# Kernel optimization log

Hardware: AMD Instinct MI355X
Metric: run time of the kernel (lower is better)

The kernel has to match this reference:

```python
import jax, jax.numpy as jnp
import numpy as np
import math

N_HEADS = 8

def setup_inputs() -> dict:
    key = jax.random.key(0)
    ks = jax.random.split(key, 5)
    B, S, D = 2, 2048, 512
    return {
        "x": jax.random.normal(ks[0], (B, S, D), dtype=jnp.float32),
        "w_in": jax.random.normal(ks[1], (3 * D, D), dtype=jnp.float32) * (1.0 / math.sqrt(D)),
        "b_in": jax.random.normal(ks[2], (3 * D,), dtype=jnp.float32) * 0.01,
        "w_out": jax.random.normal(ks[3], (D, D), dtype=jnp.float32) * (1.0 / math.sqrt(D)),
        "b_out": jax.random.normal(ks[4], (D,), dtype=jnp.float32) * 0.01,
        "casual_mask": 1,
    }

def reference(x, w_in, b_in, w_out, b_out, casual_mask):
    B, S, D = x.shape
    H = N_HEADS
    dh = D // H
    # in_proj: torch Linear -> x @ W.T + b
    qvk = x @ w_in.T + b_in  # [B, S, 3D]
    # NOTE: source unpacks as q, v, k (chunk order quirk preserved)
    q, v, k = jnp.split(qvk, 3, axis=-1)
    # [B, S, D] -> [B, H, S, dh]
    def to_heads(t):
        return t.reshape(B, S, H, dh).transpose(0, 2, 1, 3)
    q, k, v = to_heads(q), to_heads(k), to_heads(v)
    scores = jnp.einsum("bhqd,bhkd->bhqk", q, k)  # [B, H, S, S]
    if casual_mask:
        # mask BEFORE scaling, as in the source (-inf unaffected by division)
        tri = jnp.triu(jnp.ones((S, S), dtype=bool), k=1)
        scores = jnp.where(tri, -jnp.inf, scores)
    scores = scores / math.sqrt(dh)
    attn = jax.nn.softmax(scores, axis=-1)
    out = jnp.einsum("bhqk,bhkd->bhqd", attn, v)  # [B, H, S, dh]
    out = out.transpose(0, 2, 1, 3).reshape(B, S, D)
    return out @ w_out.T + b_out
```

## Files before the change

### kernel.cpp

```cpp
#include <hip/hip_runtime.h>
#include <hip/hip_bf16.h>

typedef unsigned short u16;
typedef unsigned int u32;
typedef __attribute__((ext_vector_type(8))) short bf16x8;
typedef __attribute__((ext_vector_type(4))) short bf16x4;
typedef __attribute__((ext_vector_type(4))) float f32x4;

#define DEVI __device__ __forceinline__

DEVI u16 f2bf(float f) {
  union { float f; unsigned int u; } v; v.f = f;
  unsigned int u = v.u;
  unsigned int r = (u + 0x7fffu + ((u >> 16) & 1u)) >> 16;
  return (u16)r;
}

DEVI float fexp2(float x) {
#if __has_builtin(__builtin_amdgcn_exp2f)
  return __builtin_amdgcn_exp2f(x);
#else
  return exp2f(x);
#endif
}

DEVI void lds_cp16(u16* lds, const u16* g) {
  __builtin_amdgcn_global_load_lds(
      (const __attribute__((address_space(1))) u32*)g,
      (__attribute__((address_space(3))) u32*)lds, 16, 0, 0);
}

DEVI f32x4 mfma16x16x16_bf16(bf16x4 a, bf16x4 b, f32x4 c) {
#if __has_builtin(__builtin_amdgcn_mfma_f32_16x16x16bf16_1k)
  return __builtin_amdgcn_mfma_f32_16x16x16bf16_1k(a, b, c, 0, 0, 0);
#else
  f32x4 d;
  asm volatile("v_mfma_f32_16x16x16_bf16 %0, %1, %2, %3"
               : "=v"(d) : "v"(a), "v"(b), "v"(c));
  return d;
#endif
}

__global__ __launch_bounds__(256) void cvt_all(
    const float4* __restrict__ x, const float4* __restrict__ wi,
    const float4* __restrict__ wo, u16* __restrict__ xb,
    u16* __restrict__ wib, u16* __restrict__ wob) {
  int i = blockIdx.x * 256 + threadIdx.x;
  const float4* src; u16* dst; int off;
  if (i < 524288)      { src = x;  dst = xb;  off = i; }
  else if (i < 720896) { src = wi; dst = wib; off = i - 524288; }
  else                 { src = wo; dst = wob; off = i - 720896; }
  float4 f = src[off];
  ushort4 o;
  o.x = f2bf(f.x); o.y = f2bf(f.y); o.z = f2bf(f.z); o.w = f2bf(f.w);
  ((ushort4*)dst)[off] = o;
}

__global__ __launch_bounds__(256) void inproj_gemm(
    const u16* __restrict__ xb, const u16* __restrict__ wb,
    const float* __restrict__ bin,
    u16* __restrict__ Qb, u16* __restrict__ Kb, u16* __restrict__ Vt) {
  const int K = 512;
  __shared__ u16 At[2][128 * 32];
  __shared__ u16 Bt[2][128 * 32];
  int tid = threadIdx.x;
  int w = tid >> 6, lane = tid & 63;
  int ql = lane & 15, quad = lane >> 4;
  int wr = w >> 1, wc = w & 1;
  int mtile = blockIdx.x * 128, ntile = blockIdx.y * 128;

  int r4 = lane >> 2, c4 = lane & 3;
  int swz4 = c4 ^ (r4 & 3);

  const u16* ag0 = xb + (size_t)(mtile + w * 32 + r4) * K + swz4 * 8;
  const u16* bg0 = wb + (size_t)(ntile + w * 32 + r4) * K + swz4 * 8;

  f32x4 acc[4][4];
#pragma unroll
  for (int t = 0; t < 4; ++t)
#pragma unroll
    for (int u = 0; u < 4; ++u) acc[t][u] = (f32x4){0, 0, 0, 0};

  lds_cp16(&At[0][w * 1024], ag0);
  lds_cp16(&At[0][w * 1024 + 512], ag0 + 16 * K);
  lds_cp16(&Bt[0][w * 1024], bg0);
  lds_cp16(&Bt[0][w * 1024 + 512], bg0 + 16 * K);

  int cb = ql & 3;
  for (int kk = 0; kk < 16; ++kk) {
    int cur = kk & 1;
    __syncthreads();
    if (kk < 15) {
      int k0 = (kk + 1) * 32;
      lds_cp16(&At[cur ^ 1][w * 1024], ag0 + k0);
      lds_cp16(&At[cur ^ 1][w * 1024 + 512], ag0 + 16 * K + k0);
      lds_cp16(&Bt[cur ^ 1][w * 1024], bg0 + k0);
      lds_cp16(&Bt[cur ^ 1][w * 1024 + 512], bg0 + 16 * K + k0);
    }
    bf16x8 af[4], bf[4];
#pragma unroll
    for (int t = 0; t < 4; ++t) {
      int row = wr * 64 + t * 16 + ql;
      af[t] = *(const bf16x8*)(&At[cur][row * 32 + ((quad ^ cb) * 8)]);
    }
#pragma unroll
    for (int u = 0; u < 4; ++u) {
      int row = wc * 64 + u * 16 + ql;
      bf[u] = *(const bf16x8*)(&Bt[cur][row * 32 + ((quad ^ cb) * 8)]);
    }
#pragma unroll
    for (int t = 0; t < 4; ++t)
#pragma unroll
      for (int u = 0; u < 4; ++u)
        acc[t][u] = __builtin_amdgcn_mfma_f32_16x16x32_bf16(af[t], bf[u], acc[t][u], 0, 0, 0);
  }

#pragma unroll
  for (int u = 0; u < 4; ++u) {
    int n = ntile + wc * 64 + u * 16 + ql;
    float bias = bin[n];
    int chunk = n >> 9;
    int nc = n & 511;
    int h = nc >> 6, d = nc & 63;
#pragma unroll
    for (int t = 0; t < 4; ++t)
#pragma unroll
      for (int r = 0; r < 4; ++r) {
        int m = mtile + wr * 64 + t * 16 + quad * 4 + r;
        int b = m >> 11, s = m & 2047;
        u16 val = f2bf(acc[t][u][r] + bias);
        int bh = b * 8 + h;
        if (chunk == 0)      Qb[((size_t)bh * 2048 + s) * 64 + d] = val;
        else if (chunk == 2) Kb[((size_t)bh * 2048 + s) * 64 + d] = val;
        else                 Vt[((size_t)bh * 64 + d) * 2048 + s] = val;
      }
  }
}

__global__ __launch_bounds__(512) void attn_kernel(
    const u16* __restrict__ Qb, const u16* __restrict__ Kb,
    const u16* __restrict__ Vt, u16* __restrict__ Ob) {
  const int S = 2048;
  __shared__ u16 Kt[2][2][4096];
  __shared__ u16 Vl[2][2][4096];
  int tid = threadIdx.x;
  int grp = tid >> 8;
  int w = (tid >> 6) & 3;
  int lane = tid & 63;
  int ql = lane & 15, quad = lane >> 4;
  int j = blockIdx.x;
  int tileA = j, tileB = 31 - j;
  int bh = blockIdx.y;
  int qbaseA = tileA * 64 + w * 16;
  int qbaseB = tileB * 64 + w * 16;
  const u16* Qh = Qb + (size_t)bh * S * 64;
  const u16* Kh = Kb + (size_t)bh * S * 64;
  const u16* Vh = Vt + (size_t)bh * 64 * S;

  int r8 = lane >> 3, c8 = lane & 7;
  int swz = c8 ^ r8;
  int cb = ql & 7;
  const float SCL = 0.180336878f;

  bf16x8 qA0 = *(const bf16x8*)(Qh + (size_t)(qbaseA + ql) * 64 + quad * 8);
  bf16x8 qA1 = *(const bf16x8*)(Qh + (size_t)(qbaseA + ql) * 64 + 32 + quad * 8);
  bf16x8 qB0 = *(const bf16x8*)(Qh + (size_t)(qbaseB + ql) * 64 + quad * 8);
  bf16x8 qB1 = *(const bf16x8*)(Qh + (size_t)(qbaseB + ql) * 64 + 32 + quad * 8);

  f32x4 oA[4] = {{0,0,0,0},{0,0,0,0},{0,0,0,0},{0,0,0,0}};
  f32x4 oB[4] = {{0,0,0,0},{0,0,0,0},{0,0,0,0},{0,0,0,0}};
  float mA = -3.0e38f, lA = 0.0f, mB = -3.0e38f, lB = 0.0f;

  auto stage = [&](int buf, int kbase) {
    const u16* kg = Kh + (size_t)(kbase + w * 16 + r8) * 64 + swz * 8;
    lds_cp16(&Kt[grp][buf][w * 1024], kg);
    lds_cp16(&Kt[grp][buf][w * 1024 + 512], kg + 8 * 64);
    const u16* vg = Vh + (size_t)(w * 16 + r8) * S + kbase + swz * 8;
    lds_cp16(&Vl[grp][buf][w * 1024], vg);
    lds_cp16(&Vl[grp][buf][w * 1024 + 512], vg + 8 * S);
  };
  auto process = [&](int cur, int kbase, int qbase, bf16x8 x0, bf16x8 x1,
                     f32x4 (&o)[4], float& m, float& l) {
    int q = qbase + ql;
    f32x4 st[4];
#pragma unroll
    for (int t = 0; t < 4; ++t) {
      const u16* kr = &Kt[grp][cur][(t * 16 + ql) * 64];
      bf16x8 kf0 = *(const bf16x8*)(kr + ((quad ^ cb) * 8));
      bf16x8 kf1 = *(const bf16x8*)(kr + (((quad + 4) ^ cb) * 8));
      f32x4 s = {0, 0, 0, 0};
      s = __builtin_amdgcn_mfma_f32_16x16x32_bf16(kf0, x0, s, 0, 0, 0);
      s = __builtin_amdgcn_mfma_f32_16x16x32_bf16(kf1, x1, s, 0, 0, 0);
      st[t] = s;
    }
    bool needmask = (kbase + 63 > qbase);
    float sc[4][4];
#pragma unroll
    for (int t = 0; t < 4; ++t)
#pragma unroll
      for (int r = 0; r < 4; ++r) {
        float v = st[t][r] * SCL;
        if (needmask) {
          int key = kbase + t * 16 + quad * 4 + r;
          if (key > q) v = -3.0e38f;
        }
        sc[t][r] = v;
      }
    float mx = sc[0][0];
#pragma unroll
    for (int t = 0; t < 4; ++t)
#pragma unroll
      for (int r = 0; r < 4; ++r) mx = fmaxf(mx, sc[t][r]);
    mx = fmaxf(mx, __shfl_xor(mx, 16));
    mx = fmaxf(mx, __shfl_xor(mx, 32));
    float mn = fmaxf(m, mx);
    float alpha = fexp2(m - mn);
    m = mn;
    float rs = 0.0f;
    bf16x4 p[4];
#pragma unroll
    for (int t = 0; t < 4; ++t)
#pragma unroll
      for (int r = 0; r < 4; ++r) {
        float e = fexp2(sc[t][r] - mn);
        rs += e;
        p[t][r] = (short)f2bf(e);
      }
    rs += __shfl_xor(rs, 16);
    rs += __shfl_xor(rs, 32);
    l = l * alpha + rs;
#pragma unroll
    for (int d = 0; d < 4; ++d) o[d] *= alpha;
#pragma unroll
    for (int t = 0; t < 4; ++t)
#pragma unroll
      for (int d = 0; d < 4; ++d) {
        const u16* vr = &Vl[grp][cur][(d * 16 + ql) * 64];
        bf16x4 vf = *(const bf16x4*)(vr + (((t * 2 + (quad >> 1)) ^ cb) * 8 + (quad & 1) * 4));
        o[d] = mfma16x16x16_bf16(vf, p[t], o[d]);
      }
  };

  {
    int i0 = grp * 17;
    int kb = (i0 <= tileA) ? i0 : (i0 - tileA - 1);
    stage(0, kb * 64);
  }

  for (int r = 0; r < 17; ++r) {
    int i = grp * 17 + r;
    int cur = r & 1;
    __syncthreads();
    int inext = i + 1;
    if (r + 1 < 17 && inext < 33) {
      int kb = (inext <= tileA) ? inext : (inext - tileA - 1);
      stage(cur ^ 1, kb * 64);
    }
    if (i < 33) {
      if (i <= tileA) process(cur, i * 64, qbaseA, qA0, qA1, oA, mA, lA);
      else            process(cur, (i - tileA - 1) * 64, qbaseB, qB0, qB1, oB, mB, lB);
    }
  }

  float* ob  = (float*)&Kt[0][0][0];
  float* mlb = (float*)&Vl[0][0][0];
  int lg = tid & 255;
  int b = bh >> 3, h = bh & 7;
  __syncthreads();
  if (grp == 1) {
#pragma unroll
    for (int d = 0; d < 4; ++d)
#pragma unroll
      for (int r = 0; r < 4; ++r) ob[lg * 16 + d * 4 + r] = oB[d][r];
    mlb[lg * 2] = mB;
    mlb[lg * 2 + 1] = lB;
  }
  __syncthreads();
  if (grp == 0) {
    float invA = 1.0f / lA;
    size_t rowA = ((size_t)b * 2048 + qbaseA + ql) * 512 + h * 64;
#pragma unroll
    for (int d = 0; d < 4; ++d) {
      ushort4 v;
      v.x = f2bf(oA[d][0] * invA);
      v.y = f2bf(oA[d][1] * invA);
      v.z = f2bf(oA[d][2] * invA);
      v.w = f2bf(oA[d][3] * invA);
      *(ushort4*)(Ob + rowA + d * 16 + quad * 4) = v;
    }
    float mBo = mlb[lg * 2], lBo = mlb[lg * 2 + 1];
    float M = fmaxf(mB, mBo);
    float a0 = fexp2(mB - M), a1 = fexp2(mBo - M);
    float L = lB * a0 + lBo * a1;
    float inv = 1.0f / L;
    size_t rowB = ((size_t)b * 2048 + qbaseB + ql) * 512 + h * 64;
#pragma unroll
    for (int d = 0; d < 4; ++d) {
      ushort4 v;
      v.x = f2bf((oB[d][0] * a0 + ob[lg * 16 + d * 4 + 0] * a1) * inv);
      v.y = f2bf((oB[d][1] * a0 + ob[lg * 16 + d * 4 + 1] * a1) * inv);
      v.z = f2bf((oB[d][2] * a0 + ob[lg * 16 + d * 4 + 2] * a1) * inv);
      v.w = f2bf((oB[d][3] * a0 + ob[lg * 16 + d * 4 + 3] * a1) * inv);
      *(ushort4*)(Ob + rowB + d * 16 + quad * 4) = v;
    }
  }
}

__global__ __launch_bounds__(256) void outproj_gemm(
    const u16* __restrict__ Ob, const u16* __restrict__ wb,
    const float* __restrict__ bout, float* __restrict__ out) {
  const int K = 512;
  __shared__ u16 At[2][64 * 32];
  __shared__ u16 Bt[2][128 * 32];
  int tid = threadIdx.x;
  int w = tid >> 6, lane = tid & 63;
  int ql = lane & 15, quad = lane >> 4;
  int wr = w >> 1, wc = w & 1;
  int mtile = blockIdx.x * 64, ntile = blockIdx.y * 128;

  int r4 = lane >> 2, c4 = lane & 3;
  int swz4 = c4 ^ (r4 & 3);

  const u16* ag0 = Ob + (size_t)(mtile + w * 16 + r4) * K + swz4 * 8;
  const u16* bg0 = wb + (size_t)(ntile + w * 32 + r4) * K + swz4 * 8;

  f32x4 acc[2][4];
#pragma unroll
  for (int t = 0; t < 2; ++t)
#pragma unroll
    for (int u = 0; u < 4; ++u) acc[t][u] = (f32x4){0, 0, 0, 0};

  lds_cp16(&At[0][w * 512], ag0);
  lds_cp16(&Bt[0][w * 1024], bg0);
  lds_cp16(&Bt[0][w * 1024 + 512], bg0 + 16 * K);

  int cb = ql & 3;
  for (int kk = 0; kk < 16; ++kk) {
    int cur = kk & 1;
    __syncthreads();
    if (kk < 15) {
      int k0 = (kk + 1) * 32;
      lds_cp16(&At[cur ^ 1][w * 512], ag0 + k0);
      lds_cp16(&Bt[cur ^ 1][w * 1024], bg0 + k0);
      lds_cp16(&Bt[cur ^ 1][w * 1024 + 512], bg0 + 16 * K + k0);
    }
    bf16x8 af[2], bf[4];
#pragma unroll
    for (int t = 0; t < 2; ++t) {
      int row = wr * 32 + t * 16 + ql;
      af[t] = *(const bf16x8*)(&At[cur][row * 32 + ((quad ^ cb) * 8)]);
    }
#pragma unroll
    for (int u = 0; u < 4; ++u) {
      int row = wc * 64 + u * 16 + ql;
      bf[u] = *(const bf16x8*)(&Bt[cur][row * 32 + ((quad ^ cb) * 8)]);
    }
#pragma unroll
    for (int t = 0; t < 2; ++t)
#pragma unroll
      for (int u = 0; u < 4; ++u)
        acc[t][u] = __builtin_amdgcn_mfma_f32_16x16x32_bf16(af[t], bf[u], acc[t][u], 0, 0, 0);
  }

#pragma unroll
  for (int u = 0; u < 4; ++u) {
    int n = ntile + wc * 64 + u * 16 + ql;
    float bias = bout[n];
#pragma unroll
    for (int t = 0; t < 2; ++t)
#pragma unroll
      for (int r = 0; r < 4; ++r) {
        int mm = mtile + wr * 32 + t * 16 + quad * 4 + r;
        out[(size_t)mm * 512 + n] = acc[t][u][r] + bias;
      }
  }
}

extern "C" void kernel_launch(void* const* d_in, const int* in_sizes, int n_in,
                              void* d_out, int out_size, void* d_ws, size_t ws_size,
                              hipStream_t stream) {
  const float* x     = (const float*)d_in[0];
  const float* w_in  = (const float*)d_in[1];
  const float* b_in  = (const float*)d_in[2];
  const float* w_out = (const float*)d_in[3];
  const float* b_out = (const float*)d_in[4];
  float* out = (float*)d_out;
  char* ws = (char*)d_ws;

  u16* xb    = (u16*)(ws);
  u16* winb  = (u16*)(ws + 4194304);
  u16* woutb = (u16*)(ws + 5767168);
  u16* Qb    = (u16*)(ws + 6291456);
  u16* Kb    = (u16*)(ws + 10485760);
  u16* Vt    = (u16*)(ws + 14680064);
  u16* Ob    = (u16*)(ws + 18874368);

  cvt_all<<<3072, 256, 0, stream>>>((const float4*)x, (const float4*)w_in,
                                    (const float4*)w_out, xb, winb, woutb);
  inproj_gemm<<<dim3(32, 12), 256, 0, stream>>>(xb, winb, b_in, Qb, Kb, Vt);
  attn_kernel<<<dim3(16, 16), 512, 0, stream>>>(Qb, Kb, Vt, Ob);
  outproj_gemm<<<dim3(64, 4), 256, 0, stream>>>(Ob, woutb, b_out, out);
}
```

Before: 135.9 us.

## Split attention KV range into three chunks with separate merge kernel

The attention kernel previously used 512-thread blocks, with two wave groups splitting 33 key tiles and merging through LDS. Now each block of 256 threads handles 11 key tiles for one of three chunks. Unnormalized partial outputs go to a workspace in bf16 along with per-row max and sum, and a new attn_merge kernel combines them. This triples the grid from 256 blocks to 768 to fill more CUs, at the cost of extra global traffic, a bf16 rounding of the partials and one more kernel launch.

```diff
diff --git a/kernel.cpp b/kernel.cpp
--- a/kernel.cpp
+++ b/kernel.cpp
@@ -14,6 +14,11 @@
   unsigned int u = v.u;
   unsigned int r = (u + 0x7fffu + ((u >> 16) & 1u)) >> 16;
   return (u16)r;
+}
+
+DEVI float bf2f(u16 b) {
+  union { unsigned int u; float f; } v; v.u = ((unsigned int)b) << 16;
+  return v.f;
 }
 
 DEVI float fexp2(float x) {
@@ -137,20 +142,19 @@
   }
 }
 
-__global__ __launch_bounds__(512) void attn_kernel(
+__global__ __launch_bounds__(256) void attn_kernel(
     const u16* __restrict__ Qb, const u16* __restrict__ Kb,
-    const u16* __restrict__ Vt, u16* __restrict__ Ob) {
+    const u16* __restrict__ Vt, u16* __restrict__ Pp, float* __restrict__ Ml) {
   const int S = 2048;
-  __shared__ u16 Kt[2][2][4096];
-  __shared__ u16 Vl[2][2][4096];
+  __shared__ u16 Kt[2][4096];
+  __shared__ u16 Vl[2][4096];
   int tid = threadIdx.x;
-  int grp = tid >> 8;
-  int w = (tid >> 6) & 3;
-  int lane = tid & 63;
+  int w = tid >> 6, lane = tid & 63;
   int ql = lane & 15, quad = lane >> 4;
   int j = blockIdx.x;
+  int c = blockIdx.y;
+  int bh = blockIdx.z;
   int tileA = j, tileB = 31 - j;
-  int bh = blockIdx.y;
   int qbaseA = tileA * 64 + w * 16;
   int qbaseB = tileB * 64 + w * 16;
   const u16* Qh = Qb + (size_t)bh * S * 64;
@@ -171,13 +175,14 @@
   f32x4 oB[4] = {{0,0,0,0},{0,0,0,0},{0,0,0,0},{0,0,0,0}};
   float mA = -3.0e38f, lA = 0.0f, mB = -3.0e38f, lB = 0.0f;
 
+  auto kbOf = [&](int i) { return (i <= j) ? i : (i - j - 1); };
   auto stage = [&](int buf, int kbase) {
     const u16* kg = Kh + (size_t)(kbase + w * 16 + r8) * 64 + swz * 8;
-    lds_cp16(&Kt[grp][buf][w * 1024], kg);
-    lds_cp16(&Kt[grp][buf][w * 1024 + 512], kg + 8 * 64);
+    lds_cp16(&Kt[buf][w * 1024], kg);
+    lds_cp16(&Kt[buf][w * 1024 + 512], kg + 8 * 64);
     const u16* vg = Vh + (size_t)(w * 16 + r8) * S + kbase + swz * 8;
-    lds_cp16(&Vl[grp][buf][w * 1024], vg);
-    lds_cp16(&Vl[grp][buf][w * 1024 + 512], vg + 8 * S);
+    lds_cp16(&Vl[buf][w * 1024], vg);
+    lds_cp16(&Vl[buf][w * 1024 + 512], vg + 8 * S);
   };
   auto process = [&](int cur, int kbase, int qbase, bf16x8 x0, bf16x8 x1,
                      f32x4 (&o)[4], float& m, float& l) {
@@ -185,7 +190,7 @@
     f32x4 st[4];
 #pragma unroll
     for (int t = 0; t < 4; ++t) {
-      const u16* kr = &Kt[grp][cur][(t * 16 + ql) * 64];
+      const u16* kr = &Kt[cur][(t * 16 + ql) * 64];
       bf16x8 kf0 = *(const bf16x8*)(kr + ((quad ^ cb) * 8));
       bf16x8 kf1 = *(const bf16x8*)(kr + (((quad + 4) ^ cb) * 8));
       f32x4 s = {0, 0, 0, 0};
@@ -235,75 +240,106 @@
     for (int t = 0; t < 4; ++t)
 #pragma unroll
       for (int d = 0; d < 4; ++d) {
-        const u16* vr = &Vl[grp][cur][(d * 16 + ql) * 64];
+        const u16* vr = &Vl[cur][(d * 16 + ql) * 64];
         bf16x4 vf = *(const bf16x4*)(vr + (((t * 2 + (quad >> 1)) ^ cb) * 8 + (quad & 1) * 4));
         o[d] = mfma16x16x16_bf16(vf, p[t], o[d]);
       }
   };
 
-  {
-    int i0 = grp * 17;
-    int kb = (i0 <= tileA) ? i0 : (i0 - tileA - 1);
-    stage(0, kb * 64);
-  }
-
-  for (int r = 0; r < 17; ++r) {
-    int i = grp * 17 + r;
+  stage(0, kbOf(c * 11) * 64);
+
+  for (int r = 0; r < 11; ++r) {
+    int i = c * 11 + r;
     int cur = r & 1;
     __syncthreads();
-    int inext = i + 1;
-    if (r + 1 < 17 && inext < 33) {
-      int kb = (inext <= tileA) ? inext : (inext - tileA - 1);
-      stage(cur ^ 1, kb * 64);
-    }
-    if (i < 33) {
-      if (i <= tileA) process(cur, i * 64, qbaseA, qA0, qA1, oA, mA, lA);
-      else            process(cur, (i - tileA - 1) * 64, qbaseB, qB0, qB1, oB, mB, lB);
-    }
-  }
-
-  float* ob  = (float*)&Kt[0][0][0];
-  float* mlb = (float*)&Vl[0][0][0];
-  int lg = tid & 255;
-  int b = bh >> 3, h = bh & 7;
-  __syncthreads();
-  if (grp == 1) {
-#pragma unroll
-    for (int d = 0; d < 4; ++d)
-#pragma unroll
-      for (int r = 0; r < 4; ++r) ob[lg * 16 + d * 4 + r] = oB[d][r];
-    mlb[lg * 2] = mB;
-    mlb[lg * 2 + 1] = lB;
-  }
-  __syncthreads();
-  if (grp == 0) {
-    float invA = 1.0f / lA;
-    size_t rowA = ((size_t)b * 2048 + qbaseA + ql) * 512 + h * 64;
-#pragma unroll
-    for (int d = 0; d < 4; ++d) {
+    if (r < 10) stage(cur ^ 1, kbOf(i + 1) * 64);
+    if (i <= j) process(cur, i * 64, qbaseA, qA0, qA1, oA, mA, lA);
+    else        process(cur, (i - j - 1) * 64, qbaseB, qB0, qB1, oB, mB, lB);
+  }
+
+  int qrow = w * 16 + ql;
+  size_t pb = ((((size_t)c * 16 + bh) * 16 + j) * 2) * 4096;
+  size_t mb = ((((size_t)c * 16 + bh) * 16 + j) * 2) * 128;
+  if (quad == 0) {
+    Ml[mb + qrow * 2]     = mA;
+    Ml[mb + qrow * 2 + 1] = lA;
+    Ml[mb + 128 + qrow * 2]     = mB;
+    Ml[mb + 128 + qrow * 2 + 1] = lB;
+  }
+  bool validA = (c * 11 <= j);
+  bool validB = (c * 11 + 10 > j);
+  if (validA) {
+#pragma unroll
+    for (int dt = 0; dt < 4; ++dt) {
       ushort4 v;
-      v.x = f2bf(oA[d][0] * invA);
-      v.y = f2bf(oA[d][1] * invA);
-      v.z = f2bf(oA[d][2] * invA);
-      v.w = f2bf(oA[d][3] * invA);
-      *(ushort4*)(Ob + rowA + d * 16 + quad * 4) = v;
-    }
-    float mBo = mlb[lg * 2], lBo = mlb[lg * 2 + 1];
-    float M = fmaxf(mB, mBo);
-    float a0 = fexp2(mB - M), a1 = fexp2(mBo - M);
-    float L = lB * a0 + lBo * a1;
-    float inv = 1.0f / L;
-    size_t rowB = ((size_t)b * 2048 + qbaseB + ql) * 512 + h * 64;
-#pragma unroll
-    for (int d = 0; d < 4; ++d) {
+      v.x = f2bf(oA[dt][0]); v.y = f2bf(oA[dt][1]);
+      v.z = f2bf(oA[dt][2]); v.w = f2bf(oA[dt][3]);
+      *(ushort4*)(Pp + pb + qrow * 64 + dt * 16 + quad * 4) = v;
+    }
+  }
+  if (validB) {
+#pragma unroll
+    for (int dt = 0; dt < 4; ++dt) {
       ushort4 v;
-      v.x = f2bf((oB[d][0] * a0 + ob[lg * 16 + d * 4 + 0] * a1) * inv);
-      v.y = f2bf((oB[d][1] * a0 + ob[lg * 16 + d * 4 + 1] * a1) * inv);
-      v.z = f2bf((oB[d][2] * a0 + ob[lg * 16 + d * 4 + 2] * a1) * inv);
-      v.w = f2bf((oB[d][3] * a0 + ob[lg * 16 + d * 4 + 3] * a1) * inv);
-      *(ushort4*)(Ob + rowB + d * 16 + quad * 4) = v;
-    }
-  }
+      v.x = f2bf(oB[dt][0]); v.y = f2bf(oB[dt][1]);
+      v.z = f2bf(oB[dt][2]); v.w = f2bf(oB[dt][3]);
+      *(ushort4*)(Pp + pb + 4096 + qrow * 64 + dt * 16 + quad * 4) = v;
+    }
+  }
+}
+
+__global__ __launch_bounds__(256) void attn_merge(
+    const u16* __restrict__ Pp, const float* __restrict__ Ml,
+    u16* __restrict__ Ob) {
+  int tid = threadIdx.x;
+  int j = blockIdx.x, t = blockIdx.y, bh = blockIdx.z;
+  int q = tid >> 2, ds = (tid & 3) * 16;
+  float mc[3], lc[3];
+#pragma unroll
+  for (int c = 0; c < 3; ++c) {
+    size_t mb = ((((size_t)c * 16 + bh) * 16 + j) * 2 + t) * 128 + q * 2;
+    mc[c] = Ml[mb]; lc[c] = Ml[mb + 1];
+  }
+  float M = -3.0e38f;
+#pragma unroll
+  for (int c = 0; c < 3; ++c)
+    if (lc[c] > 0.0f) M = fmaxf(M, mc[c]);
+  float L = 0.0f, wgt[3];
+#pragma unroll
+  for (int c = 0; c < 3; ++c) {
+    wgt[c] = (lc[c] > 0.0f) ? fexp2(mc[c] - M) : 0.0f;
+    L += lc[c] * wgt[c];
+  }
+  float O[16];
+#pragma unroll
+  for (int i = 0; i < 16; ++i) O[i] = 0.0f;
+#pragma unroll
+  for (int c = 0; c < 3; ++c) {
+    if (lc[c] > 0.0f) {
+      size_t pb = ((((size_t)c * 16 + bh) * 16 + j) * 2 + t) * 4096 + q * 64 + ds;
+      union { bf16x8 v; u16 e[8]; } a, b;
+      a.v = *(const bf16x8*)(Pp + pb);
+      b.v = *(const bf16x8*)(Pp + pb + 8);
+#pragma unroll
+      for (int i = 0; i < 8; ++i) {
+        O[i]     += wgt[c] * bf2f(a.e[i]);
+        O[i + 8] += wgt[c] * bf2f(b.e[i]);
+      }
+    }
+  }
+  float inv = 1.0f / L;
+  int tile_abs = t ? (31 - j) : j;
+  int s = tile_abs * 64 + q;
+  int b2 = bh >> 3, h = bh & 7;
+  size_t row = ((size_t)(b2 * 2048 + s)) * 512 + h * 64 + ds;
+  union { bf16x8 v; u16 e[8]; } o0, o1;
+#pragma unroll
+  for (int i = 0; i < 8; ++i) {
+    o0.e[i] = f2bf(O[i] * inv);
+    o1.e[i] = f2bf(O[i + 8] * inv);
+  }
+  *(bf16x8*)(Ob + row)     = o0.v;
+  *(bf16x8*)(Ob + row + 8) = o1.v;
 }
 
 __global__ __launch_bounds__(256) void outproj_gemm(
@@ -394,10 +430,13 @@
   u16* Kb    = (u16*)(ws + 10485760);
   u16* Vt    = (u16*)(ws + 14680064);
   u16* Ob    = (u16*)(ws + 18874368);
+  u16* Pp    = (u16*)(ws + 23068672);
+  float* Ml  = (float*)(ws + 35651584);
 
   cvt_all<<<3072, 256, 0, stream>>>((const float4*)x, (const float4*)w_in,
                                     (const float4*)w_out, xb, winb, woutb);
   inproj_gemm<<<dim3(32, 12), 256, 0, stream>>>(xb, winb, b_in, Qb, Kb, Vt);
-  attn_kernel<<<dim3(16, 16), 512, 0, stream>>>(Qb, Kb, Vt, Ob);
+  attn_kernel<<<dim3(16, 3, 16), 256, 0, stream>>>(Qb, Kb, Vt, Pp, Ml);
+  attn_merge<<<dim3(16, 2, 16), 256, 0, stream>>>(Pp, Ml, Ob);
   outproj_gemm<<<dim3(64, 4), 256, 0, stream>>>(Ob, woutb, b_out, out);
 }
```

Result: slower. 143.0 us (+5.2%).
